# Kernel optimization log

Hardware: AMD Instinct MI355X
Metric: run time of the kernel (lower is better)

The kernel has to match this reference:

```python
import jax, jax.numpy as jnp
import numpy as np

H = W = 2048
TANH_C = 1.1486328125  # probability-correction constant from the model
DEG2RAD = np.float32(np.pi / 180.0)

# Fire-spread direction angle (degrees, East=0, counterclockwise) from the
# neighbor at 3x3 window position (r, c) toward the center cell.
DIR_DEG = jnp.array([[315., 270., 225.],
                     [  0.,   0., 180.],
                     [ 45.,  90., 135.]], dtype=jnp.float32)
CENTER_MASK = jnp.ones((3, 3), jnp.float32).at[1, 1].set(0.0)  # exclude self


def _neighborhood(x):
    """x: [H,W] -> [H,W,3,3] with [i,j,r,c] = x[i+r-1, j+c-1], zero padded."""
    xp = jnp.pad(x, 1)
    return jnp.stack(
        [jnp.stack([xp[r:r + H, c:c + W] for c in range(3)], axis=-1)
         for r in range(3)], axis=-2)


def setup_inputs() -> dict:
    key = jax.random.key(0)
    ks = jax.random.split(key, 8)
    p_veg = jax.random.uniform(ks[0], (H, W), jnp.float32)
    p_den = jax.random.uniform(ks[1], (H, W), jnp.float32)
    wind_velocity = jax.random.uniform(ks[2], (H, W), jnp.float32) * 10.0
    wind_towards_direction = jax.random.uniform(ks[3], (H, W), jnp.float32) * 360.0
    slope = (jax.random.uniform(ks[4], (H, W, 3, 3), jnp.float32) - 0.5) * 60.0
    burning = jax.random.uniform(ks[5], (H, W)) < 0.01  # sparse initial ignition
    burned = jnp.zeros((H, W), dtype=bool)
    rand_ignite = jax.random.uniform(ks[6], (H, W), jnp.float32)
    rand_continue = jax.random.uniform(ks[7], (H, W), jnp.float32)
    return dict(
        p_veg=p_veg, p_den=p_den,
        wind_velocity=wind_velocity, wind_towards_direction=wind_towards_direction,
        slope=slope,
        a=jnp.float32(0.1), p_h=jnp.float32(0.3),
        c_1=jnp.float32(0.1), c_2=jnp.float32(0.1), p_continue=jnp.float32(0.3),
        rand_ignite=rand_ignite, rand_continue=rand_continue,
        burning=burning, burned=burned,
    )


def reference(p_veg, p_den, wind_velocity, wind_towards_direction, slope,
              a, p_h, c_1, c_2, p_continue,
              rand_ignite, rand_continue, burning, burned):
    # p_w = exp(c1*V) * exp(c2*V*(cos(theta_w)-1)), theta_w = angle between
    # wind direction and per-neighbor spread direction. [H,W,3,3]
    theta_w = (wind_towards_direction[..., None, None] - DIR_DEG) * DEG2RAD
    p_w = (jnp.exp(c_1 * wind_velocity)[..., None, None]
           * jnp.exp(c_2 * wind_velocity[..., None, None] * (jnp.cos(theta_w) - 1.0)))
    # p_s = exp(a * theta_s), slope angle in radians. [H,W,3,3]
    p_s = jnp.exp(a * slope * DEG2RAD)
    # p_propagate = tanh(c * p_h*(1+p_veg)*(1+p_den)*p_w*p_s)
    p_base = p_h * (1.0 + p_veg) * (1.0 + p_den)  # [H,W]
    p_prop = jnp.tanh(TANH_C * (p_base[..., None, None] * p_w * p_s))
    # 8-neighbor burning indicators (center masked out). [H,W,3,3]
    nbr_burning = _neighborhood(burning.astype(jnp.float32)) * CENTER_MASK
    # p_ignite = 1 - prod_j (1 - p_propagate_j * burning_j)
    p_ignite = 1.0 - jnp.prod(1.0 - p_prop * nbr_burning, axis=(-2, -1))
    # Stochastic state transition.
    burnable = ~burning & ~burned
    new_ignited = burnable & (rand_ignite < p_ignite)
    keep = burning & (rand_continue < p_continue)
    new_burning = new_ignited | keep
    new_burned = burned | (burning & ~keep)
    return p_ignite, jnp.stack([new_burning, new_burned])
```

## Files before the change

### kernel.cpp

```cpp
#include <hip/hip_runtime.h>
#include <math.h>

namespace {

constexpr int H = 2048;
constexpr int W = 2048;
constexpr float TANH_C  = 1.1486328125f;
constexpr float DEG2RAD = 0.017453292519943295f;
constexpr float RT2H    = 0.70710678118654752f;
constexpr float BAND    = 2.5e-4f;

__global__ __launch_bounds__(256) void wildfire_step(
    const float* __restrict__ p_veg,  const float* __restrict__ p_den,
    const float* __restrict__ wind_v, const float* __restrict__ wind_d,
    const float* __restrict__ slope,
    const float* __restrict__ s_a,  const float* __restrict__ s_ph,
    const float* __restrict__ s_c1, const float* __restrict__ s_c2,
    const float* __restrict__ s_pc,
    const float* __restrict__ rand_ig, const float* __restrict__ rand_co,
    const int* __restrict__ burning, const int* __restrict__ burned,
    float* __restrict__ out)
{
    __shared__ float sb[3][260];
    const int t  = (int)threadIdx.x;
    const int i  = (int)blockIdx.y;
    const int j0 = (int)blockIdx.x * 256;
    const int j  = j0 + t;

    for (int r = 0; r < 3; ++r) {
        const int ii = i + r - 1;
        for (int c = t; c < 258; c += 256) {
            const int jj = j0 - 1 + c;
            float v = 0.f;
            if (ii >= 0 && ii < H && jj >= 0 && jj < W)
                v = burning[ii * W + jj] ? 1.f : 0.f;
            sb[r][c] = v;
        }
    }
    __syncthreads();

    const float b0 = sb[0][t], b1 = sb[0][t+1], b2 = sb[0][t+2];
    const float b3 = sb[1][t], bc = sb[1][t+1], b5 = sb[1][t+2];
    const float b6 = sb[2][t], b7 = sb[2][t+1], b8 = sb[2][t+2];

    const int   idx        = i * W + j;
    const bool  is_burning = (bc != 0.f);
    const int   was_burned = burned[idx];
    const float rco        = rand_co[idx];
    const float p_cont     = s_pc[0];

    const float any_n = b0 + b1 + b2 + b3 + b5 + b6 + b7 + b8;

    float p_ignite    = 0.f;
    bool  new_ignited = false;

    if (__any(any_n != 0.f)) {
        const float pv  = p_veg[idx];
        const float pd  = p_den[idx];
        const float wv  = wind_v[idx];
        const float wd  = wind_d[idx];
        const float rig = rand_ig[idx];
        float sl[9];
        __builtin_memcpy(sl, slope + (size_t)idx * 9, 9 * sizeof(float));

        const float a   = s_a[0];
        const float p_h = s_ph[0];
        const float c1  = s_c1[0];
        const float c2  = s_c2[0];

        const float wr  = wd * DEG2RAD;
        const float cw  = __cosf(wr);
        const float sw  = __sinf(wr);
        const float ew  = __expf(c1 * wv);
        const float cvw = c2 * wv;
        const float asl = a * DEG2RAD;
        const float p_base = (p_h * (1.f + pv)) * (1.f + pd);
        const float Cz2 = 2.f * (TANH_C * (p_base * ew));

#define NB(K, b, CK, SK, si)                                                \
        const float ct##K = fmaf(cw, (CK), sw * (SK));                      \
        const float eu##K = __expf(fmaf(cvw, ct##K - 1.f, asl * sl[si]));   \
        const float E##K  = __expf(Cz2 * eu##K);                            \
        const float d##K  = fmaf((b), E##K, 1.f);

        NB(0, b0,  RT2H, -RT2H, 0)
        NB(1, b1,  0.f,  -1.f,  1)
        NB(2, b2, -RT2H, -RT2H, 2)
        NB(3, b3,  1.f,   0.f,  3)
        NB(5, b5, -1.f,   0.f,  5)
        NB(6, b6,  RT2H,  RT2H, 6)
        NB(7, b7,  0.f,   1.f,  7)
        NB(8, b8, -RT2H,  RT2H, 8)
#undef NB
        const float den = ((d0 * d1) * (d2 * d3)) * ((d5 * d6) * (d7 * d8));
        const float num = (float)(1 << (int)any_n);
        p_ignite = 1.f - num * __builtin_amdgcn_rcpf(den);

        new_ignited = (!is_burning) && (was_burned == 0) && (rig < p_ignite);

        const bool need = (any_n != 0.f) && (fabsf(rig - p_ignite) < BAND);
        if (__any((int)need)) {
            if (need) {
                const float ewp = expf(c1 * wv);
                float prod = 1.f;
#define NBP(b, dirdeg, si)                                                  \
                if ((b) != 0.f) {                                           \
                    const float th = (wd - (dirdeg)) * DEG2RAD;             \
                    const float pw = ewp * expf(cvw * (cosf(th) - 1.f));    \
                    const float ps = expf((a * sl[si]) * DEG2RAD);          \
                    const float pp = tanhf(TANH_C * ((p_base * pw) * ps));  \
                    prod *= 1.f - pp * (b);                                 \
                }
                NBP(b0, 315.f, 0)
                NBP(b1, 270.f, 1)
                NBP(b2, 225.f, 2)
                NBP(b3,   0.f, 3)
                NBP(b5, 180.f, 5)
                NBP(b6,  45.f, 6)
                NBP(b7,  90.f, 7)
                NBP(b8, 135.f, 8)
#undef NBP
                p_ignite    = 1.f - prod;
                new_ignited = (!is_burning) && (was_burned == 0) && (rig < p_ignite);
            }
        }
    }

    const bool keep = is_burning && (rco < p_cont);
    const bool nb   = new_ignited || keep;
    const bool nd   = (was_burned != 0) || (is_burning && !keep);

    out[idx]             = p_ignite;
    out[H * W + idx]     = nb ? 1.f : 0.f;
    out[2 * H * W + idx] = nd ? 1.f : 0.f;
}

}

extern "C" void kernel_launch(void* const* d_in, const int* in_sizes, int n_in,
                              void* d_out, int out_size, void* d_ws, size_t ws_size,
                              hipStream_t stream)
{
    (void)in_sizes; (void)n_in; (void)out_size; (void)d_ws; (void)ws_size;
    dim3 grid(W / 256, H, 1);
    dim3 block(256, 1, 1);
    hipLaunchKernelGGL(wildfire_step, grid, block, 0, stream,
        (const float*)d_in[0],  (const float*)d_in[1],
        (const float*)d_in[2],  (const float*)d_in[3],
        (const float*)d_in[4],
        (const float*)d_in[5],  (const float*)d_in[6],
        (const float*)d_in[7],  (const float*)d_in[8],
        (const float*)d_in[9],
        (const float*)d_in[10], (const float*)d_in[11],
        (const int*)d_in[12],   (const int*)d_in[13],
        (float*)d_out);
}
```

Baseline: 328.4 us.

## Process four rows per block with a shared halo and upfront loads

Each block now handles four output rows, so the burning halo tile covers six rows instead of three per row, cutting redundant halo loads. All per-cell inputs, including the nine slope values for each of the four rows, are issued before the barrier so memory latency overlaps. Loads are no longer skipped when a wavefront has no burning neighbors, so input traffic becomes unconditional. The larger register footprint is paired with a launch bound of two blocks per SM, which may limit occupancy.

After: 338.2 us. +3.0%, slower.

```diff
diff --git a/kernel.cpp b/kernel.cpp
--- a/kernel.cpp
+++ b/kernel.cpp
@@ -5,12 +5,13 @@
 
 constexpr int H = 2048;
 constexpr int W = 2048;
+constexpr int ROWS = 4;
 constexpr float TANH_C  = 1.1486328125f;
 constexpr float DEG2RAD = 0.017453292519943295f;
 constexpr float RT2H    = 0.70710678118654752f;
 constexpr float BAND    = 2.5e-4f;
 
-__global__ __launch_bounds__(256) void wildfire_step(
+__global__ __launch_bounds__(256, 2) void wildfire_step(
     const float* __restrict__ p_veg,  const float* __restrict__ p_den,
     const float* __restrict__ wind_v, const float* __restrict__ wind_d,
     const float* __restrict__ slope,
@@ -21,118 +22,143 @@
     const int* __restrict__ burning, const int* __restrict__ burned,
     float* __restrict__ out)
 {
-    __shared__ float sb[3][260];
+    __shared__ float sb[ROWS + 2][260];
     const int t  = (int)threadIdx.x;
-    const int i  = (int)blockIdx.y;
+    const int i0 = (int)blockIdx.y * ROWS;
     const int j0 = (int)blockIdx.x * 256;
     const int j  = j0 + t;
 
-    for (int r = 0; r < 3; ++r) {
-        const int ii = i + r - 1;
-        for (int c = t; c < 258; c += 256) {
-            const int jj = j0 - 1 + c;
-            float v = 0.f;
-            if (ii >= 0 && ii < H && jj >= 0 && jj < W)
-                v = burning[ii * W + jj] ? 1.f : 0.f;
-            sb[r][c] = v;
+    float ha[ROWS + 2], hbx[ROWS + 2];
+    #pragma unroll
+    for (int r = 0; r < ROWS + 2; ++r) {
+        const int ii = i0 - 1 + r;
+        const int jj = j0 - 1 + t;
+        float v = 0.f;
+        if (ii >= 0 && ii < H && jj >= 0) v = burning[ii * W + jj] ? 1.f : 0.f;
+        ha[r] = v;
+        float v2 = 0.f;
+        if (t < 2) {
+            const int jj2 = j0 + 255 + t;
+            if (ii >= 0 && ii < H && jj2 < W) v2 = burning[ii * W + jj2] ? 1.f : 0.f;
         }
+        hbx[r] = v2;
+    }
+
+    float pv[ROWS], pd[ROWS], wvl[ROWS], wdl[ROWS], rig[ROWS], rco[ROWS];
+    int   bd[ROWS];
+    float sl[ROWS][9];
+    #pragma unroll
+    for (int r = 0; r < ROWS; ++r) {
+        const int idx = (i0 + r) * W + j;
+        pv[r]  = p_veg[idx];
+        pd[r]  = p_den[idx];
+        wvl[r] = wind_v[idx];
+        wdl[r] = wind_d[idx];
+        rig[r] = rand_ig[idx];
+        rco[r] = rand_co[idx];
+        bd[r]  = burned[idx];
+        __builtin_memcpy(sl[r], slope + (size_t)idx * 9, 9 * sizeof(float));
+    }
+
+    const float a      = s_a[0];
+    const float p_h    = s_ph[0];
+    const float c1     = s_c1[0];
+    const float c2     = s_c2[0];
+    const float p_cont = s_pc[0];
+
+    #pragma unroll
+    for (int r = 0; r < ROWS + 2; ++r) {
+        sb[r][t] = ha[r];
+        if (t < 2) sb[r][256 + t] = hbx[r];
     }
     __syncthreads();
 
-    const float b0 = sb[0][t], b1 = sb[0][t+1], b2 = sb[0][t+2];
-    const float b3 = sb[1][t], bc = sb[1][t+1], b5 = sb[1][t+2];
-    const float b6 = sb[2][t], b7 = sb[2][t+1], b8 = sb[2][t+2];
+    float wA[ROWS + 2], wB[ROWS + 2], wC[ROWS + 2];
+    #pragma unroll
+    for (int r = 0; r < ROWS + 2; ++r) {
+        wA[r] = sb[r][t]; wB[r] = sb[r][t + 1]; wC[r] = sb[r][t + 2];
+    }
 
-    const int   idx        = i * W + j;
-    const bool  is_burning = (bc != 0.f);
-    const int   was_burned = burned[idx];
-    const float rco        = rand_co[idx];
-    const float p_cont     = s_pc[0];
+    #pragma unroll
+    for (int r = 0; r < ROWS; ++r) {
+        const float b0 = wA[r],     b1 = wB[r],     b2 = wC[r];
+        const float b3 = wA[r + 1], bcn = wB[r + 1], b5 = wC[r + 1];
+        const float b6 = wA[r + 2], b7 = wB[r + 2], b8 = wC[r + 2];
 
-    const float any_n = b0 + b1 + b2 + b3 + b5 + b6 + b7 + b8;
+        const int   idx        = (i0 + r) * W + j;
+        const bool  is_burning = (bcn != 0.f);
+        const float any_n = b0 + b1 + b2 + b3 + b5 + b6 + b7 + b8;
 
-    float p_ignite    = 0.f;
-    bool  new_ignited = false;
+        float p_ig   = 0.f;
+        bool  new_ig = false;
 
-    if (__any(any_n != 0.f)) {
-        const float pv  = p_veg[idx];
-        const float pd  = p_den[idx];
-        const float wv  = wind_v[idx];
-        const float wd  = wind_d[idx];
-        const float rig = rand_ig[idx];
-        float sl[9];
-        __builtin_memcpy(sl, slope + (size_t)idx * 9, 9 * sizeof(float));
+        if (__any(any_n != 0.f)) {
+            const float wr  = wdl[r] * DEG2RAD;
+            const float cw  = __cosf(wr);
+            const float sw  = __sinf(wr);
+            const float ew  = __expf(c1 * wvl[r]);
+            const float cvw = c2 * wvl[r];
+            const float asl = a * DEG2RAD;
+            const float p_base = (p_h * (1.f + pv[r])) * (1.f + pd[r]);
+            const float Cz2 = 2.f * (TANH_C * (p_base * ew));
 
-        const float a   = s_a[0];
-        const float p_h = s_ph[0];
-        const float c1  = s_c1[0];
-        const float c2  = s_c2[0];
+#define NB(K, b, CK, SK, si)                                                  \
+            const float ct##K = fmaf(cw, (CK), sw * (SK));                    \
+            const float eu##K = __expf(fmaf(cvw, ct##K - 1.f, asl * sl[r][si])); \
+            const float E##K  = __expf(Cz2 * eu##K);                          \
+            const float d##K  = fmaf((b), E##K, 1.f);
 
-        const float wr  = wd * DEG2RAD;
-        const float cw  = __cosf(wr);
-        const float sw  = __sinf(wr);
-        const float ew  = __expf(c1 * wv);
-        const float cvw = c2 * wv;
-        const float asl = a * DEG2RAD;
-        const float p_base = (p_h * (1.f + pv)) * (1.f + pd);
-        const float Cz2 = 2.f * (TANH_C * (p_base * ew));
+            NB(0, b0,  RT2H, -RT2H, 0)
+            NB(1, b1,  0.f,  -1.f,  1)
+            NB(2, b2, -RT2H, -RT2H, 2)
+            NB(3, b3,  1.f,   0.f,  3)
+            NB(5, b5, -1.f,   0.f,  5)
+            NB(6, b6,  RT2H,  RT2H, 6)
+            NB(7, b7,  0.f,   1.f,  7)
+            NB(8, b8, -RT2H,  RT2H, 8)
+#undef NB
+            const float den = ((d0 * d1) * (d2 * d3)) * ((d5 * d6) * (d7 * d8));
+            const float num = (float)(1 << (int)any_n);
+            p_ig = 1.f - num * __builtin_amdgcn_rcpf(den);
 
-#define NB(K, b, CK, SK, si)                                                \
-        const float ct##K = fmaf(cw, (CK), sw * (SK));                      \
-        const float eu##K = __expf(fmaf(cvw, ct##K - 1.f, asl * sl[si]));   \
-        const float E##K  = __expf(Cz2 * eu##K);                            \
-        const float d##K  = fmaf((b), E##K, 1.f);
+            new_ig = (!is_burning) && (bd[r] == 0) && (rig[r] < p_ig);
 
-        NB(0, b0,  RT2H, -RT2H, 0)
-        NB(1, b1,  0.f,  -1.f,  1)
-        NB(2, b2, -RT2H, -RT2H, 2)
-        NB(3, b3,  1.f,   0.f,  3)
-        NB(5, b5, -1.f,   0.f,  5)
-        NB(6, b6,  RT2H,  RT2H, 6)
-        NB(7, b7,  0.f,   1.f,  7)
-        NB(8, b8, -RT2H,  RT2H, 8)
-#undef NB
-        const float den = ((d0 * d1) * (d2 * d3)) * ((d5 * d6) * (d7 * d8));
-        const float num = (float)(1 << (int)any_n);
-        p_ignite = 1.f - num * __builtin_amdgcn_rcpf(den);
-
-        new_ignited = (!is_burning) && (was_burned == 0) && (rig < p_ignite);
-
-        const bool need = (any_n != 0.f) && (fabsf(rig - p_ignite) < BAND);
-        if (__any((int)need)) {
-            if (need) {
-                const float ewp = expf(c1 * wv);
-                float prod = 1.f;
-#define NBP(b, dirdeg, si)                                                  \
-                if ((b) != 0.f) {                                           \
-                    const float th = (wd - (dirdeg)) * DEG2RAD;             \
-                    const float pw = ewp * expf(cvw * (cosf(th) - 1.f));    \
-                    const float ps = expf((a * sl[si]) * DEG2RAD);          \
-                    const float pp = tanhf(TANH_C * ((p_base * pw) * ps));  \
-                    prod *= 1.f - pp * (b);                                 \
+            const bool need = (any_n != 0.f) && (fabsf(rig[r] - p_ig) < BAND);
+            if (__any((int)need)) {
+                if (need) {
+                    const float ewp = expf(c1 * wvl[r]);
+                    float prod = 1.f;
+#define NBP(b, dirdeg, si)                                                    \
+                    if ((b) != 0.f) {                                         \
+                        const float th = (wdl[r] - (dirdeg)) * DEG2RAD;       \
+                        const float pw = ewp * expf(cvw * (cosf(th) - 1.f));  \
+                        const float ps = expf((a * sl[r][si]) * DEG2RAD);     \
+                        const float pp = tanhf(TANH_C * ((p_base * pw) * ps)); \
+                        prod *= 1.f - pp * (b);                               \
+                    }
+                    NBP(b0, 315.f, 0)
+                    NBP(b1, 270.f, 1)
+                    NBP(b2, 225.f, 2)
+                    NBP(b3,   0.f, 3)
+                    NBP(b5, 180.f, 5)
+                    NBP(b6,  45.f, 6)
+                    NBP(b7,  90.f, 7)
+                    NBP(b8, 135.f, 8)
+#undef NBP
+                    p_ig   = 1.f - prod;
+                    new_ig = (!is_burning) && (bd[r] == 0) && (rig[r] < p_ig);
                 }
-                NBP(b0, 315.f, 0)
-                NBP(b1, 270.f, 1)
-                NBP(b2, 225.f, 2)
-                NBP(b3,   0.f, 3)
-                NBP(b5, 180.f, 5)
-                NBP(b6,  45.f, 6)
-                NBP(b7,  90.f, 7)
-                NBP(b8, 135.f, 8)
-#undef NBP
-                p_ignite    = 1.f - prod;
-                new_ignited = (!is_burning) && (was_burned == 0) && (rig < p_ignite);
             }
         }
+
+        const bool keep = is_burning && (rco[r] < p_cont);
+        const bool nb   = new_ig || keep;
+        const bool nd   = (bd[r] != 0) || (is_burning && !keep);
+
+        out[idx]             = p_ig;
+        out[H * W + idx]     = nb ? 1.f : 0.f;
+        out[2 * H * W + idx] = nd ? 1.f : 0.f;
     }
-
-    const bool keep = is_burning && (rco < p_cont);
-    const bool nb   = new_ignited || keep;
-    const bool nd   = (was_burned != 0) || (is_burning && !keep);
-
-    out[idx]             = p_ignite;
-    out[H * W + idx]     = nb ? 1.f : 0.f;
-    out[2 * H * W + idx] = nd ? 1.f : 0.f;
 }
 
 }
@@ -142,7 +168,7 @@
                               hipStream_t stream)
 {
     (void)in_sizes; (void)n_in; (void)out_size; (void)d_ws; (void)ws_size;
-    dim3 grid(W / 256, H, 1);
+    dim3 grid(W / 256, H / ROWS, 1);
     dim3 block(256, 1, 1);
     hipLaunchKernelGGL(wildfire_step, grid, block, 0, stream,
         (const float*)d_in[0],  (const float*)d_in[1],
```
